# Performance work log

Hardware: AMD Instinct MI355X
Metric: run time of the kernel (lower is better)

## Reference

```python
import jax, jax.numpy as jnp
import numpy as np
from jax import lax

B, C, H, W = 4, 256, 64, 64
K = 9          # points
G = 32         # GroupNorm groups
EPS = 1e-5


def base_offset():
    # matches get_base_offset: y = 0, x in [-(K-1)//2 .. K//2], interleaved (y,x)
    bx = jnp.arange(-((K - 1) // 2), K // 2 + 1, dtype=jnp.float32)
    by = jnp.zeros_like(bx)
    return jnp.stack([by, bx], axis=1).reshape(1, 2 * K, 1, 1)


def conv3x3(x, w, b):
    y = lax.conv_general_dilated(x, w, (1, 1), ((1, 1), (1, 1)),
                                 dimension_numbers=('NCHW', 'OIHW', 'NCHW'))
    return y + b[None, :, None, None]


def group_norm(x, gamma, beta):
    b, c, h, w = x.shape
    xg = x.reshape(b, G, c // G, h, w)
    mu = xg.mean(axis=(2, 3, 4), keepdims=True)
    var = xg.var(axis=(2, 3, 4), keepdims=True)
    xn = ((xg - mu) * lax.rsqrt(var + EPS)).reshape(b, c, h, w)
    return xn * gamma[None, :, None, None] + beta[None, :, None, None]


def _deform_sample_one(img, off):
    # img: [C,H,W]; off: [K,2,H,W] (y,x). Kernel [1,K], stride 1, pad (0, K//2).
    c, h, w = img.shape
    base_x = (jnp.arange(K) - K // 2).astype(img.dtype)  # kernel grid x positions
    py = off[:, 0] + jnp.arange(h, dtype=img.dtype)[None, :, None]                 # [K,H,W]
    px = off[:, 1] + jnp.arange(w, dtype=img.dtype)[None, None, :] + base_x[:, None, None]
    y0 = jnp.floor(py)
    x0 = jnp.floor(px)
    wy = py - y0
    wx = px - x0
    flat = img.reshape(c, h * w)

    def corner(yi, xi):
        valid = (yi >= 0) & (yi <= h - 1) & (xi >= 0) & (xi <= w - 1)
        yc = jnp.clip(yi, 0, h - 1).astype(jnp.int32)
        xc = jnp.clip(xi, 0, w - 1).astype(jnp.int32)
        v = flat[:, (yc * w + xc).reshape(-1)].reshape(c, K, h, w)
        return v * valid[None].astype(img.dtype)

    return (corner(y0, x0) * ((1 - wy) * (1 - wx))[None]
            + corner(y0, x0 + 1) * ((1 - wy) * wx)[None]
            + corner(y0 + 1, x0) * (wy * (1 - wx))[None]
            + corner(y0 + 1, x0 + 1) * (wy * wx)[None])  # [C,K,H,W]


def deform_conv(x, offset, w):
    # x [B,C,H,W]; offset [B,2K,H,W]; w [O,C,1,K]; no bias (mmcv DeformConv2d)
    b, _, h, ww = x.shape
    off = offset.reshape(b, K, 2, h, ww)
    cols = jax.vmap(_deform_sample_one)(x, off)  # [B,C,K,H,W]
    return jnp.einsum('bckhw,ock->bohw', cols, w[:, :, 0, :])


def setup_inputs() -> dict:
    key = jax.random.key(0)
    ks = jax.random.split(key, 8)
    return {
        'cls_feat': jax.random.normal(ks[0], (B, C, H, W), jnp.float32),
        'reg_feat': jax.random.normal(ks[1], (B, C, H, W), jnp.float32),
        'offc_w': jax.random.normal(ks[2], (C, C, 3, 3), jnp.float32) * 0.01,
        'offc_b': jnp.zeros((C,), jnp.float32),
        'offc_g': jnp.ones((C,), jnp.float32),
        'offc_bt': jnp.zeros((C,), jnp.float32),
        'offo_w': jax.random.normal(ks[3], (2 * K, C, 3, 3), jnp.float32) * 0.01,
        'offo_b': jnp.zeros((2 * K,), jnp.float32),
        'clsdc_w': jax.random.normal(ks[4], (C, C, 1, K), jnp.float32) / np.sqrt(C * K),
        'cls_g': jnp.ones((C,), jnp.float32),
        'cls_bt': jnp.zeros((C,), jnp.float32),
        'regdc_w': jax.random.normal(ks[5], (C, C, 1, K), jnp.float32) / np.sqrt(C * K),
        'reg_g': jnp.ones((C,), jnp.float32),
        'reg_bt': jnp.zeros((C,), jnp.float32),
    }


def reference(cls_feat, reg_feat, offc_w, offc_b, offc_g, offc_bt,
              offo_w, offo_b, clsdc_w, cls_g, cls_bt, regdc_w, reg_g, reg_bt):
    # offset branch: ConvModule(3x3) -> GN -> ReLU, then 3x3 offset_out head
    t = jax.nn.relu(group_norm(conv3x3(reg_feat, offc_w, offc_b), offc_g, offc_bt))
    pts = conv3x3(t, offo_w, offo_b)          # [B, 2K, H, W]
    off = pts - base_offset()
    cls_out = jax.nn.relu(group_norm(deform_conv(cls_feat, off, clsdc_w), cls_g, cls_bt))
    reg_out = jax.nn.relu(group_norm(deform_conv(reg_feat, off, regdc_w), reg_g, reg_bt))
    return pts, cls_out, reg_out
```

## Files before the change

### kernel.cpp

```cpp
#include <hip/hip_runtime.h>
#include <math.h>

#define BB 4
#define CC 256
#define HH 64
#define WW 64
#define KP 9
#define GG 32
#define HWW (HH*WW)
#define FEL ((size_t)BB*CC*HH*WW)
#define GN_CNT 32768.0f

typedef __bf16 bf16x8 __attribute__((ext_vector_type(8)));
typedef float  f32x4  __attribute__((ext_vector_type(4)));
typedef float  f32x2  __attribute__((ext_vector_type(2)));

__device__ __forceinline__ float bflo(unsigned u) {
    union { unsigned u; float f; } x; x.u = u << 16; return x.f;
}
__device__ __forceinline__ float bfhi(unsigned u) {
    union { unsigned u; float f; } x; x.u = u & 0xffff0000u; return x.f;
}
__device__ __forceinline__ f32x2 up2(unsigned u) {
    return (f32x2){bflo(u), bfhi(u)};
}

#define VT256_RD(row, P)  (((row) << 8) + ((((P) ^ ((row) & 7))) << 3))
#define VT128_RD(row, P)  (((row) << 7) + ((((P) ^ ((row) & 7))) << 3))

__global__ void prep_and_transpose(
    const float* __restrict__ cls, const float* __restrict__ reg,
    __bf16* __restrict__ out_cls, __bf16* __restrict__ out_reg,
    const float* __restrict__ w1, const float* __restrict__ wc,
    const float* __restrict__ wr, const float* __restrict__ w18,
    __bf16* __restrict__ f1, __bf16* __restrict__ fc,
    __bf16* __restrict__ fr, __bf16* __restrict__ f18,
    float* __restrict__ stats)
{
    int blk = blockIdx.x;
    if (blk < 2048) {
        __shared__ float tile[64][65];
        int c0 = (blk & 3) * 64;
        int y  = (blk >> 2) & 63;
        int z  = blk >> 8;
        int b  = z & 3;
        const float* in = (z >> 2) ? reg : cls;
        __bf16* out     = (z >> 2) ? out_reg : out_cls;
        int lx = threadIdx.x & 63;
        int q  = threadIdx.x >> 6;
        for (int j = 0; j < 16; ++j) {
            int ci = q * 16 + j;
            tile[ci][lx] = in[(((size_t)b*CC + c0 + ci)*HH + y)*WW + lx];
        }
        __syncthreads();
        for (int j = 0; j < 16; ++j) {
            int xi = q * 16 + j;
            out[(((size_t)b*HH + y)*WW + xi)*CC + c0 + lx] = (__bf16)tile[lx][xi];
        }
        return;
    }
    int gid = (blk - 2048) * 256 + threadIdx.x;
    if (gid < 768) stats[gid] = 0.f;
    const int NW = 589824;
    if (gid < 3 * NW) {
        int which = gid / NW;
        int idx = gid - which * NW;
        int j   = idx & 7;
        int l   = (idx >> 3) & 63;
        int o16 = (idx >> 9) & 15;
        int c0  = (idx >> 13) & 7;
        int k   = idx >> 16;
        int o = o16 * 16 + (l & 15);
        int c = c0 * 32 + (l >> 4) * 8 + j;
        const float* src = (which == 0) ? w1 : ((which == 1) ? wc : wr);
        __bf16* dst = (which == 0) ? f1 : ((which == 1) ? fc : fr);
        dst[idx] = (__bf16)src[(size_t)(o * 256 + c) * 9 + k];
    } else {
        int idx = gid - 3 * NW;
        int j   = idx & 7;
        int l   = (idx >> 3) & 63;
        int o16 = (idx >> 9) & 1;
        int c0  = (idx >> 10) & 7;
        int k   = idx >> 13;
        int o = o16 * 16 + (l & 15);
        int c = c0 * 32 + (l >> 4) * 8 + j;
        float v = (o < 18) ? w18[(size_t)(o * 256 + c) * 9 + k] : 0.f;
        f18[idx] = (__bf16)v;
    }
}

__global__ __launch_bounds__(256, 4) void conv1_mfma(
    const __bf16* __restrict__ in_cl,
    const __bf16* __restrict__ wf,
    const float* __restrict__ bias,
    __bf16* __restrict__ t_out,
    float* __restrict__ stats)
{
    __shared__ __bf16 Vt[66 * 256];
    __shared__ float groupStats[64];
    int blk = blockIdx.x;
    int bb = blk & 3;
    int oq = (blk >> 2) & 3;
    int y  = blk >> 4;
    int t  = threadIdx.x;
    int w  = t >> 6;
    int l  = t & 63;
    int quad = l >> 4;
    int l15  = l & 15;
    if (t < 64) groupStats[t] = 0.f;

    const __bf16* inb = in_cl + (size_t)bb * HWW * CC;
    f32x4 acc[4];
    #pragma unroll
    for (int i = 0; i < 4; ++i) acc[i] = (f32x4){0.f, 0.f, 0.f, 0.f};

    for (int ky = 0; ky < 3; ++ky) {
        int yy = y + ky - 1;
        bool yok = (yy >= 0 && yy < HH);
        __syncthreads();
        for (int u = t; u < 66 * 32; u += 256) {
            int xl = u >> 5, cu = u & 31;
            int gx = xl - 1;
            uint4 val = make_uint4(0u, 0u, 0u, 0u);
            if (yok && gx >= 0 && gx < WW)
                val = *(const uint4*)(inb + ((size_t)(yy * WW + gx)) * CC + cu * 8);
            *(uint4*)&Vt[VT256_RD(xl, cu)] = val;
        }
        __syncthreads();
        #pragma unroll
        for (int kx = 0; kx < 3; ++kx) {
            int k = ky * 3 + kx;
            const bf16x8* wbase = (const bf16x8*)(wf + (size_t)k * 65536);
            for (int c0 = 0; c0 < 8; ++c0) {
                bf16x8 a[4];
                #pragma unroll
                for (int pt = 0; pt < 4; ++pt) {
                    int row = pt * 16 + l15 + kx;
                    a[pt] = *(const bf16x8*)&Vt[VT256_RD(row, c0 * 4 + quad)];
                }
                bf16x8 bfr = wbase[(c0 * 16 + (oq * 4 + w)) * 64 + l];
                #pragma unroll
                for (int pt = 0; pt < 4; ++pt)
                    acc[pt] = __builtin_amdgcn_mfma_f32_16x16x32_bf16(
                        a[pt], bfr, acc[pt], 0, 0, 0);
            }
        }
    }
    {
        int o = oq * 64 + w * 16 + l15;
        float bi = bias[o];
        float s1 = 0.f, s2 = 0.f;
        #pragma unroll
        for (int pt = 0; pt < 4; ++pt)
            #pragma unroll
            for (int r = 0; r < 4; ++r) {
                float v = acc[pt][r] + bi;
                int px = pt * 16 + quad * 4 + r;
                t_out[(((size_t)bb * HH + y) * WW + px) * CC + o] = (__bf16)v;
                s1 += v; s2 += v * v;
            }
        s1 += __shfl_xor(s1, 16, 64); s1 += __shfl_xor(s1, 32, 64);
        s2 += __shfl_xor(s2, 16, 64); s2 += __shfl_xor(s2, 32, 64);
        if (quad == 0) {
            atomicAdd(&groupStats[(o >> 3) * 2],     s1);
            atomicAdd(&groupStats[(o >> 3) * 2 + 1], s2);
        }
    }
    __syncthreads();
    if (t < 64) atomicAdd(&stats[bb * 64 + t], groupStats[t]);
}

__global__ __launch_bounds__(256, 4) void conv18_mfma(
    const __bf16* __restrict__ t_bf,
    const __bf16* __restrict__ wf18,
    const float* __restrict__ bias,
    const float* __restrict__ stats,
    const float* __restrict__ gamma, const float* __restrict__ beta,
    float* __restrict__ pts)
{
    __shared__ __bf16 Vt[34 * 256];
    int blk = blockIdx.x;
    int bb = blk & 3;
    int xh = (blk >> 2) & 1;
    int y  = blk >> 3;
    int t  = threadIdx.x;
    int w  = t >> 6;
    int l  = t & 63;
    int quad = l >> 4;
    int l15  = l & 15;
    int mt   = w & 1;
    int o16  = w >> 1;
    int x0   = xh * 32;
    const __bf16* inb = t_bf + (size_t)bb * HWW * CC;

    int cu = t & 31;
    int cbase = cu * 8;
    float mu = stats[bb * 64 + cu * 2]     * (1.f / GN_CNT);
    float ms = stats[bb * 64 + cu * 2 + 1] * (1.f / GN_CNT);
    float rs = rsqrtf(ms - mu * mu + 1e-5f);
    float sc[8], sh[8];
    #pragma unroll
    for (int j = 0; j < 8; ++j) {
        float ga = gamma[cbase + j];
        sc[j] = rs * ga;
        sh[j] = beta[cbase + j] - mu * rs * ga;
    }

    f32x4 acc = (f32x4){0.f, 0.f, 0.f, 0.f};

    for (int ky = 0; ky < 3; ++ky) {
        int yy = y + ky - 1;
        bool yok = (yy >= 0 && yy < HH);
        __syncthreads();
        for (int u = t; u < 34 * 32; u += 256) {
            int xl = u >> 5;
            int gx = x0 - 1 + xl;
            uint4 val = make_uint4(0u, 0u, 0u, 0u);
            if (yok && gx >= 0 && gx < WW) {
                uint4 q = *(const uint4*)(inb + ((size_t)(yy * WW + gx)) * CC + cu * 8);
                __bf16 o8[8];
                unsigned qq[4] = {q.x, q.y, q.z, q.w};
                #pragma unroll
                for (int h = 0; h < 4; ++h) {
                    float lo = fmaxf(bflo(qq[h]) * sc[h*2]   + sh[h*2],   0.f);
                    float hi = fmaxf(bfhi(qq[h]) * sc[h*2+1] + sh[h*2+1], 0.f);
                    o8[h*2]   = (__bf16)lo;
                    o8[h*2+1] = (__bf16)hi;
                }
                val = *(const uint4*)o8;
            }
            *(uint4*)&Vt[VT256_RD(xl, cu)] = val;
        }
        __syncthreads();
        #pragma unroll
        for (int kx = 0; kx < 3; ++kx) {
            int k = ky * 3 + kx;
            const bf16x8* wbase = (const bf16x8*)(wf18 + (size_t)k * 8192);
            for (int c0 = 0; c0 < 8; ++c0) {
                int row = mt * 16 + l15 + kx;
                bf16x8 a = *(const bf16x8*)&Vt[VT256_RD(row, c0 * 4 + quad)];
                bf16x8 bfr = wbase[(c0 * 2 + o16) * 64 + l];
                acc = __builtin_amdgcn_mfma_f32_16x16x32_bf16(a, bfr, acc, 0, 0, 0);
            }
        }
    }
    {
        int o = o16 * 16 + l15;
        if (o < 18) {
            float bi = bias[o];
            float4 st;
            st.x = acc[0] + bi;
            st.y = acc[1] + bi;
            st.z = acc[2] + bi;
            st.w = acc[3] + bi;
            *(float4*)(pts + (((size_t)bb*18 + o)*HH + y)*WW + x0 + mt*16 + quad*4) = st;
        }
    }
}

__global__ __launch_bounds__(512, 4) void deform_mfma(
    const __bf16* __restrict__ cls_cl, const __bf16* __restrict__ reg_cl,
    const __bf16* __restrict__ wfc, const __bf16* __restrict__ wfr,
    const float* __restrict__ pts,
    __bf16* __restrict__ out_cls, __bf16* __restrict__ out_reg,
    float* __restrict__ stats)
{
    __shared__ float pairW4[576 * 4];
    __shared__ int   pairO4[576 * 4];
    __shared__ __bf16 Vt[2][64 * 128];
    __shared__ float groupStats[64];

    int blk = blockIdx.x;
    int g8  = blk & 7;
    int which = g8 & 1;
    int bb  = g8 >> 1;
    int y   = blk >> 3;
    const __bf16* featb = (which ? reg_cl : cls_cl) + (size_t)bb * HWW * CC;
    const __bf16* wf    = which ? wfr : wfc;
    __bf16* outp  = which ? out_reg : out_cls;
    float* statsP = stats + 256 + which * 256 + bb * 64;

    int t = threadIdx.x;
    int w = t >> 6;
    int l = t & 63;
    int quad = l >> 4;
    int l15  = l & 15;
    int cq4  = t & 15;
    int pxg  = t >> 4;

    if (t < 64) groupStats[t] = 0.f;
    for (int j = t; j < 576; j += 512) {
        int k = j >> 6;
        int x = j & 63;
        float py  = pts[(((size_t)bb*18 + 2*k)*HH + y)*WW + x] + (float)y;
        float pxf = pts[(((size_t)bb*18 + 2*k + 1)*HH + y)*WW + x] + (float)x;
        float y0f = floorf(py), x0f = floorf(pxf);
        float wy = py - y0f, wx = pxf - x0f;
        int iy0 = (int)y0f, ix0 = (int)x0f;
        int iy1 = iy0 + 1,  ix1 = ix0 + 1;
        bool vy0 = (iy0 >= 0 && iy0 < HH), vy1 = (iy1 >= 0 && iy1 < HH);
        bool vx0 = (ix0 >= 0 && ix0 < WW), vx1 = (ix1 >= 0 && ix1 < WW);
        int cy0 = min(max(iy0, 0), HH-1), cy1 = min(max(iy1, 0), HH-1);
        int cx0 = min(max(ix0, 0), WW-1), cx1 = min(max(ix1, 0), WW-1);
        pairW4[j*4+0] = (1.f-wy)*(1.f-wx) * ((vy0 && vx0) ? 1.f : 0.f);
        pairW4[j*4+1] = (1.f-wy)*wx       * ((vy0 && vx1) ? 1.f : 0.f);
        pairW4[j*4+2] = wy*(1.f-wx)       * ((vy1 && vx0) ? 1.f : 0.f);
        pairW4[j*4+3] = wy*wx             * ((vy1 && vx1) ? 1.f : 0.f);
        pairO4[j*4+0] = (cy0*WW + cx0)*CC;
        pairO4[j*4+1] = (cy0*WW + cx1)*CC;
        pairO4[j*4+2] = (cy1*WW + cx0)*CC;
        pairO4[j*4+3] = (cy1*WW + cx1)*CC;
    }

    f32x4 acc[2][4];
    #pragma unroll
    for (int i = 0; i < 2; ++i)
        #pragma unroll
        for (int j = 0; j < 4; ++j)
            acc[i][j] = (f32x4){0.f, 0.f, 0.f, 0.f};

    uint4 L[2][4];

    auto gathers = [&](int s) {
        int k = s >> 1, ch = s & 1;
        const __bf16* fb = featb + ch * 128 + cq4 * 8;
        #pragma unroll
        for (int it = 0; it < 2; ++it) {
            int j = k * 64 + it * 32 + pxg;
            int4 ov = *(const int4*)&pairO4[j * 4];
            L[it][0] = *(const uint4*)(fb + ov.x);
            L[it][1] = *(const uint4*)(fb + ov.y);
            L[it][2] = *(const uint4*)(fb + ov.z);
            L[it][3] = *(const uint4*)(fb + ov.w);
        }
    };
    auto combine = [&](int s) {
        __bf16* buf = &Vt[s & 1][0];
        int k = s >> 1;
        #pragma unroll
        for (int it = 0; it < 2; ++it) {
            int pxi = it * 32 + pxg;
            float4 wv = *(const float4*)&pairW4[(k * 64 + pxi) * 4];
            __bf16 o8[8];
            unsigned q0[4] = {L[it][0].x, L[it][0].y, L[it][0].z, L[it][0].w};
            unsigned q1[4] = {L[it][1].x, L[it][1].y, L[it][1].z, L[it][1].w};
            unsigned q2[4] = {L[it][2].x, L[it][2].y, L[it][2].z, L[it][2].w};
            unsigned q3[4] = {L[it][3].x, L[it][3].y, L[it][3].z, L[it][3].w};
            #pragma unroll
            for (int h = 0; h < 4; ++h) {
                f32x2 r = wv.x * up2(q0[h]);
                r += wv.y * up2(q1[h]);
                r += wv.z * up2(q2[h]);
                r += wv.w * up2(q3[h]);
                o8[h*2]   = (__bf16)r.x;
                o8[h*2+1] = (__bf16)r.y;
            }
            *(uint4*)&buf[VT128_RD(pxi, cq4)] = *(const uint4*)o8;
        }
    };
    auto stage_mfma = [&](int s) {
        int ch = s & 1;
        const __bf16* buf = &Vt[s & 1][0];
        const bf16x8* wbase = (const bf16x8*)(wf + (size_t)(s >> 1) * 65536);
        #pragma unroll
        for (int u = 0; u < 4; ++u) {
            bf16x8 a[4], bfr[2];
            #pragma unroll
            for (int pt = 0; pt < 4; ++pt)
                a[pt] = *(const bf16x8*)&buf[VT128_RD(pt * 16 + l15, u * 4 + quad)];
            #pragma unroll
            for (int ot = 0; ot < 2; ++ot)
                bfr[ot] = wbase[(((ch * 4 + u) * 16) + (w * 2 + ot)) * 64 + l];
            #pragma unroll
            for (int ot = 0; ot < 2; ++ot)
                #pragma unroll
                for (int pt = 0; pt < 4; ++pt)
                    acc[ot][pt] = __builtin_amdgcn_mfma_f32_16x16x32_bf16(
                        bfr[ot], a[pt], acc[ot][pt], 0, 0, 0);
        }
    };

    __syncthreads();
    gathers(0);
    combine(0);
    #pragma unroll 1
    for (int s = 1; s < 18; ++s) {
        __syncthreads();
        gathers(s);
        stage_mfma(s - 1);
        combine(s);
    }
    __syncthreads();
    stage_mfma(17);

    #pragma unroll
    for (int ot = 0; ot < 2; ++ot) {
        float s1 = 0.f, s2 = 0.f;
        #pragma unroll
        for (int r = 0; r < 4; ++r) {
            int o = w * 32 + ot * 16 + quad * 4 + r;
            __bf16* orow = outp + ((size_t)(bb*CC + o))*HWW + y*WW + l15;
            #pragma unroll
            for (int pt = 0; pt < 4; ++pt) {
                float v = acc[ot][pt][r];
                orow[pt * 16] = (__bf16)v;
                s1 += v; s2 += v * v;
            }
        }
        s1 += __shfl_xor(s1, 1, 64); s1 += __shfl_xor(s1, 2, 64);
        s1 += __shfl_xor(s1, 4, 64); s1 += __shfl_xor(s1, 8, 64);
        s1 += __shfl_xor(s1, 16, 64);
        s2 += __shfl_xor(s2, 1, 64); s2 += __shfl_xor(s2, 2, 64);
        s2 += __shfl_xor(s2, 4, 64); s2 += __shfl_xor(s2, 8, 64);
        s2 += __shfl_xor(s2, 16, 64);
        if ((l & 31) == 0) {
            int g = w * 4 + ot * 2 + (l >> 5);
            atomicAdd(&groupStats[g * 2],     s1);
            atomicAdd(&groupStats[g * 2 + 1], s2);
        }
    }
    __syncthreads();
    if (t < 64) atomicAdd(&statsP[t], groupStats[t]);
}

__global__ void gn_relu_nchw(const __bf16* __restrict__ in_cls, const __bf16* __restrict__ in_reg,
                             float* __restrict__ out_cls, float* __restrict__ out_reg,
                             const float* __restrict__ stats_base,
                             const float* __restrict__ gcls, const float* __restrict__ bcls,
                             const float* __restrict__ greg, const float* __restrict__ breg) {
    int which = blockIdx.y;
    const __bf16* in = which ? in_reg  : in_cls;
    float* out       = which ? out_reg : out_cls;
    const float* st  = stats_base + (which ? 512 : 256);
    const float* gg  = which ? greg : gcls;
    const float* be  = which ? breg : bcls;
    size_t e = ((size_t)blockIdx.x * 256 + threadIdx.x) * 8;
    int c = (int)((e >> 12) & 255);
    int b = (int)(e >> 20);
    int g = c >> 3;
    float mu = st[(b*32 + g)*2] * (1.f / GN_CNT);
    float ms = st[(b*32 + g)*2 + 1] * (1.f / GN_CNT);
    float rs = rsqrtf(ms - mu*mu + 1e-5f);
    float ga = gg[c], bb = be[c];
    uint4 q = *(const uint4*)(in + e);
    float v[8] = {bflo(q.x), bfhi(q.x), bflo(q.y), bfhi(q.y),
                  bflo(q.z), bfhi(q.z), bflo(q.w), bfhi(q.w)};
    float4 r0, r1;
    r0.x = fmaxf((v[0] - mu)*rs*ga + bb, 0.f);
    r0.y = fmaxf((v[1] - mu)*rs*ga + bb, 0.f);
    r0.z = fmaxf((v[2] - mu)*rs*ga + bb, 0.f);
    r0.w = fmaxf((v[3] - mu)*rs*ga + bb, 0.f);
    r1.x = fmaxf((v[4] - mu)*rs*ga + bb, 0.f);
    r1.y = fmaxf((v[5] - mu)*rs*ga + bb, 0.f);
    r1.z = fmaxf((v[6] - mu)*rs*ga + bb, 0.f);
    r1.w = fmaxf((v[7] - mu)*rs*ga + bb, 0.f);
    *(float4*)(out + e)     = r0;
    *(float4*)(out + e + 4) = r1;
}

extern "C" void kernel_launch(void* const* d_in, const int* in_sizes, int n_in,
                              void* d_out, int out_size, void* d_ws, size_t ws_size,
                              hipStream_t stream) {
    (void)in_sizes; (void)n_in; (void)out_size; (void)ws_size;
    const float* cls_feat = (const float*)d_in[0];
    const float* reg_feat = (const float*)d_in[1];
    const float* offc_w   = (const float*)d_in[2];
    const float* offc_b   = (const float*)d_in[3];
    const float* offc_g   = (const float*)d_in[4];
    const float* offc_bt  = (const float*)d_in[5];
    const float* offo_w   = (const float*)d_in[6];
    const float* offo_b   = (const float*)d_in[7];
    const float* clsdc_w  = (const float*)d_in[8];
    const float* cls_g    = (const float*)d_in[9];
    const float* cls_bt   = (const float*)d_in[10];
    const float* regdc_w  = (const float*)d_in[11];
    const float* reg_g    = (const float*)d_in[12];
    const float* reg_bt   = (const float*)d_in[13];
    float* out = (float*)d_out;

    char* ws = (char*)d_ws;
    __bf16* reg_cl = (__bf16*)ws;
    __bf16* cls_cl = (__bf16*)(ws + 8388608);
    __bf16* t_bf   = (__bf16*)(ws + 16777216);
    __bf16* dc_cls = (__bf16*)(ws + 25165824);
    __bf16* dc_reg = (__bf16*)(ws + 33554432);
    __bf16* wt1f   = (__bf16*)(ws + 41943040);
    __bf16* wtcf   = (__bf16*)(ws + 41943040 + 1179648);
    __bf16* wtrf   = (__bf16*)(ws + 41943040 + 2359296);
    __bf16* wf18   = (__bf16*)(ws + 41943040 + 3538944);
    float*  stats  = (float*)(ws + 41943040 + 3686400);

    float* pts     = out;
    float* out_cls = out + 294912;
    float* out_reg = out + 294912 + FEL;

    hipLaunchKernelGGL(prep_and_transpose, dim3(9248), dim3(256), 0, stream,
                       cls_feat, reg_feat, cls_cl, reg_cl,
                       offc_w, clsdc_w, regdc_w, offo_w,
                       wt1f, wtcf, wtrf, wf18, stats);
    hipLaunchKernelGGL(conv1_mfma, dim3(1024), dim3(256), 0, stream,
                       reg_cl, wt1f, offc_b, t_bf, stats);
    hipLaunchKernelGGL(conv18_mfma, dim3(512), dim3(256), 0, stream,
                       t_bf, wf18, offo_b, stats, offc_g, offc_bt, pts);
    hipLaunchKernelGGL(deform_mfma, dim3(512), dim3(512), 0, stream,
                       cls_cl, reg_cl, wtcf, wtrf, pts, dc_cls, dc_reg, stats);
    hipLaunchKernelGGL(gn_relu_nchw, dim3(2048, 2), dim3(256), 0, stream,
                       dc_cls, dc_reg, out_cls, out_reg,
                       stats, cls_g, cls_bt, reg_g, reg_bt);
}
```

Before: 230.4 us.

## Widen conv1 and deform blocks to cover all channels and two rows

Measured after the change: 239.8 us. 4.1% more time.

```diff
diff --git a/kernel.cpp b/kernel.cpp
--- a/kernel.cpp
+++ b/kernel.cpp
@@ -89,7 +89,7 @@
     }
 }
 
-__global__ __launch_bounds__(256, 4) void conv1_mfma(
+__global__ __launch_bounds__(512, 2) void conv1_mfma(
     const __bf16* __restrict__ in_cl,
     const __bf16* __restrict__ wf,
     const float* __restrict__ bias,
@@ -100,8 +100,7 @@
     __shared__ float groupStats[64];
     int blk = blockIdx.x;
     int bb = blk & 3;
-    int oq = (blk >> 2) & 3;
-    int y  = blk >> 4;
+    int y  = blk >> 2;
     int t  = threadIdx.x;
     int w  = t >> 6;
     int l  = t & 63;
@@ -110,15 +109,18 @@
     if (t < 64) groupStats[t] = 0.f;
 
     const __bf16* inb = in_cl + (size_t)bb * HWW * CC;
-    f32x4 acc[4];
+    f32x4 acc[4][2];
     #pragma unroll
-    for (int i = 0; i < 4; ++i) acc[i] = (f32x4){0.f, 0.f, 0.f, 0.f};
+    for (int i = 0; i < 4; ++i)
+        #pragma unroll
+        for (int j = 0; j < 2; ++j)
+            acc[i][j] = (f32x4){0.f, 0.f, 0.f, 0.f};
 
     for (int ky = 0; ky < 3; ++ky) {
         int yy = y + ky - 1;
         bool yok = (yy >= 0 && yy < HH);
         __syncthreads();
-        for (int u = t; u < 66 * 32; u += 256) {
+        for (int u = t; u < 66 * 32; u += 512) {
             int xl = u >> 5, cu = u & 31;
             int gx = xl - 1;
             uint4 val = make_uint4(0u, 0u, 0u, 0u);
@@ -132,29 +134,34 @@
             int k = ky * 3 + kx;
             const bf16x8* wbase = (const bf16x8*)(wf + (size_t)k * 65536);
             for (int c0 = 0; c0 < 8; ++c0) {
-                bf16x8 a[4];
+                bf16x8 a[4], bfr[2];
                 #pragma unroll
                 for (int pt = 0; pt < 4; ++pt) {
                     int row = pt * 16 + l15 + kx;
                     a[pt] = *(const bf16x8*)&Vt[VT256_RD(row, c0 * 4 + quad)];
                 }
-                bf16x8 bfr = wbase[(c0 * 16 + (oq * 4 + w)) * 64 + l];
+                #pragma unroll
+                for (int ot = 0; ot < 2; ++ot)
+                    bfr[ot] = wbase[(c0 * 16 + (w * 2 + ot)) * 64 + l];
                 #pragma unroll
                 for (int pt = 0; pt < 4; ++pt)
-                    acc[pt] = __builtin_amdgcn_mfma_f32_16x16x32_bf16(
-                        a[pt], bfr, acc[pt], 0, 0, 0);
-            }
-        }
-    }
-    {
-        int o = oq * 64 + w * 16 + l15;
+                    #pragma unroll
+                    for (int ot = 0; ot < 2; ++ot)
+                        acc[pt][ot] = __builtin_amdgcn_mfma_f32_16x16x32_bf16(
+                            a[pt], bfr[ot], acc[pt][ot], 0, 0, 0);
+            }
+        }
+    }
+    #pragma unroll
+    for (int ot = 0; ot < 2; ++ot) {
+        int o = w * 32 + ot * 16 + l15;
         float bi = bias[o];
         float s1 = 0.f, s2 = 0.f;
         #pragma unroll
         for (int pt = 0; pt < 4; ++pt)
             #pragma unroll
             for (int r = 0; r < 4; ++r) {
-                float v = acc[pt][r] + bi;
+                float v = acc[pt][ot][r] + bi;
                 int px = pt * 16 + quad * 4 + r;
                 t_out[(((size_t)bb * HH + y) * WW + px) * CC + o] = (__bf16)v;
                 s1 += v; s2 += v * v;
@@ -258,23 +265,23 @@
     }
 }
 
-__global__ __launch_bounds__(512, 4) void deform_mfma(
+__global__ __launch_bounds__(1024, 1) void deform_mfma(
     const __bf16* __restrict__ cls_cl, const __bf16* __restrict__ reg_cl,
     const __bf16* __restrict__ wfc, const __bf16* __restrict__ wfr,
     const float* __restrict__ pts,
     __bf16* __restrict__ out_cls, __bf16* __restrict__ out_reg,
     float* __restrict__ stats)
 {
-    __shared__ float pairW4[576 * 4];
-    __shared__ int   pairO4[576 * 4];
-    __shared__ __bf16 Vt[2][64 * 128];
+    __shared__ float pairW4[1152 * 4];
+    __shared__ int   pairO4[1152 * 4];
+    __shared__ __bf16 Vt[2][128 * 128];
     __shared__ float groupStats[64];
 
     int blk = blockIdx.x;
     int g8  = blk & 7;
     int which = g8 & 1;
     int bb  = g8 >> 1;
-    int y   = blk >> 3;
+    int y0  = (blk >> 3) * 2;
     const __bf16* featb = (which ? reg_cl : cls_cl) + (size_t)bb * HWW * CC;
     const __bf16* wf    = which ? wfr : wfc;
     __bf16* outp  = which ? out_reg : out_cls;
@@ -286,12 +293,17 @@
     int quad = l >> 4;
     int l15  = l & 15;
     int cq4  = t & 15;
-    int pxg  = t >> 4;
+    int sg   = t >> 4;
+    int ow   = w & 7;
+    int rh   = w >> 3;
 
     if (t < 64) groupStats[t] = 0.f;
-    for (int j = t; j < 576; j += 512) {
-        int k = j >> 6;
-        int x = j & 63;
+    for (int j = t; j < 1152; j += 1024) {
+        int k = j >> 7;
+        int site = j & 127;
+        int r = site >> 6;
+        int x = site & 63;
+        int y = y0 + r;
         float py  = pts[(((size_t)bb*18 + 2*k)*HH + y)*WW + x] + (float)y;
         float pxf = pts[(((size_t)bb*18 + 2*k + 1)*HH + y)*WW + x] + (float)x;
         float y0f = floorf(py), x0f = floorf(pxf);
@@ -326,7 +338,7 @@
         const __bf16* fb = featb + ch * 128 + cq4 * 8;
         #pragma unroll
         for (int it = 0; it < 2; ++it) {
-            int j = k * 64 + it * 32 + pxg;
+            int j = k * 128 + it * 64 + sg;
             int4 ov = *(const int4*)&pairO4[j * 4];
             L[it][0] = *(const uint4*)(fb + ov.x);
             L[it][1] = *(const uint4*)(fb + ov.y);
@@ -339,8 +351,8 @@
         int k = s >> 1;
         #pragma unroll
         for (int it = 0; it < 2; ++it) {
-            int pxi = it * 32 + pxg;
-            float4 wv = *(const float4*)&pairW4[(k * 64 + pxi) * 4];
+            int site = it * 64 + sg;
+            float4 wv = *(const float4*)&pairW4[(k * 128 + site) * 4];
             __bf16 o8[8];
             unsigned q0[4] = {L[it][0].x, L[it][0].y, L[it][0].z, L[it][0].w};
             unsigned q1[4] = {L[it][1].x, L[it][1].y, L[it][1].z, L[it][1].w};
@@ -355,7 +367,7 @@
                 o8[h*2]   = (__bf16)r.x;
                 o8[h*2+1] = (__bf16)r.y;
             }
-            *(uint4*)&buf[VT128_RD(pxi, cq4)] = *(const uint4*)o8;
+            *(uint4*)&buf[VT128_RD(site, cq4)] = *(const uint4*)o8;
         }
     };
     auto stage_mfma = [&](int s) {
@@ -366,11 +378,13 @@
         for (int u = 0; u < 4; ++u) {
             bf16x8 a[4], bfr[2];
             #pragma unroll
-            for (int pt = 0; pt < 4; ++pt)
-                a[pt] = *(const bf16x8*)&buf[VT128_RD(pt * 16 + l15, u * 4 + quad)];
+            for (int pt = 0; pt < 4; ++pt) {
+                int row = rh * 64 + pt * 16 + l15;
+                a[pt] = *(const bf16x8*)&buf[VT128_RD(row, u * 4 + quad)];
+            }
             #pragma unroll
             for (int ot = 0; ot < 2; ++ot)
-                bfr[ot] = wbase[(((ch * 4 + u) * 16) + (w * 2 + ot)) * 64 + l];
+                bfr[ot] = wbase[(((ch * 4 + u) * 16) + (ow * 2 + ot)) * 64 + l];
             #pragma unroll
             for (int ot = 0; ot < 2; ++ot)
                 #pragma unroll
@@ -398,8 +412,8 @@
         float s1 = 0.f, s2 = 0.f;
         #pragma unroll
         for (int r = 0; r < 4; ++r) {
-            int o = w * 32 + ot * 16 + quad * 4 + r;
-            __bf16* orow = outp + ((size_t)(bb*CC + o))*HWW + y*WW + l15;
+            int o = ow * 32 + ot * 16 + quad * 4 + r;
+            __bf16* orow = outp + ((size_t)(bb*CC + o))*HWW + (y0 + rh)*WW + l15;
             #pragma unroll
             for (int pt = 0; pt < 4; ++pt) {
                 float v = acc[ot][pt][r];
@@ -414,7 +428,7 @@
         s2 += __shfl_xor(s2, 4, 64); s2 += __shfl_xor(s2, 8, 64);
         s2 += __shfl_xor(s2, 16, 64);
         if ((l & 31) == 0) {
-            int g = w * 4 + ot * 2 + (l >> 5);
+            int g = ow * 4 + ot * 2 + (l >> 5);
             atomicAdd(&groupStats[g * 2],     s1);
             atomicAdd(&groupStats[g * 2 + 1], s2);
         }
@@ -498,11 +512,11 @@
                        cls_feat, reg_feat, cls_cl, reg_cl,
                        offc_w, clsdc_w, regdc_w, offo_w,
                        wt1f, wtcf, wtrf, wf18, stats);
-    hipLaunchKernelGGL(conv1_mfma, dim3(1024), dim3(256), 0, stream,
+    hipLaunchKernelGGL(conv1_mfma, dim3(256), dim3(512), 0, stream,
                        reg_cl, wt1f, offc_b, t_bf, stats);
     hipLaunchKernelGGL(conv18_mfma, dim3(512), dim3(256), 0, stream,
                        t_bf, wf18, offo_b, stats, offc_g, offc_bt, pts);
-    hipLaunchKernelGGL(deform_mfma, dim3(512), dim3(512), 0, stream,
+    hipLaunchKernelGGL(deform_mfma, dim3(256), dim3(1024), 0, stream,
                        cls_cl, reg_cl, wtcf, wtrf, pts, dc_cls, dc_reg, stats);
     hipLaunchKernelGGL(gn_relu_nchw, dim3(2048, 2), dim3(256), 0, stream,
                        dc_cls, dc_reg, out_cls, out_reg,
```

## Retile conv1 MFMA warps to 2x2 pixel/output tiles and widen LDS swizzle

Applied to the files above, without the earlier changes.

New measurement: 233.3 us. Within noise of the previous version (+1.2%).

```diff
diff --git a/kernel.cpp b/kernel.cpp
--- a/kernel.cpp
+++ b/kernel.cpp
@@ -25,8 +25,8 @@
     return (f32x2){bflo(u), bfhi(u)};
 }
 
-#define VT256_RD(row, P)  (((row) << 8) + ((((P) ^ ((row) & 7))) << 3))
-#define VT128_RD(row, P)  (((row) << 7) + ((((P) ^ ((row) & 7))) << 3))
+#define VT256_RD(row, P)  (((row) << 8) + ((((P) ^ ((row) & 15))) << 3))
+#define VT128_RD(row, P)  (((row) << 7) + ((((P) ^ ((row) & 15))) << 3))
 
 __global__ void prep_and_transpose(
     const float* __restrict__ cls, const float* __restrict__ reg,
@@ -107,12 +107,17 @@
     int l  = t & 63;
     int quad = l >> 4;
     int l15  = l & 15;
+    int ph  = w & 1;
+    int oh2 = w >> 1;
     if (t < 64) groupStats[t] = 0.f;
 
     const __bf16* inb = in_cl + (size_t)bb * HWW * CC;
-    f32x4 acc[4];
+    f32x4 acc[2][2];
     #pragma unroll
-    for (int i = 0; i < 4; ++i) acc[i] = (f32x4){0.f, 0.f, 0.f, 0.f};
+    for (int i = 0; i < 2; ++i)
+        #pragma unroll
+        for (int j = 0; j < 2; ++j)
+            acc[i][j] = (f32x4){0.f, 0.f, 0.f, 0.f};
 
     for (int ky = 0; ky < 3; ++ky) {
         int yy = y + ky - 1;
@@ -132,30 +137,35 @@
             int k = ky * 3 + kx;
             const bf16x8* wbase = (const bf16x8*)(wf + (size_t)k * 65536);
             for (int c0 = 0; c0 < 8; ++c0) {
-                bf16x8 a[4];
+                bf16x8 a[2], bfr[2];
                 #pragma unroll
-                for (int pt = 0; pt < 4; ++pt) {
-                    int row = pt * 16 + l15 + kx;
+                for (int pt = 0; pt < 2; ++pt) {
+                    int row = ph * 32 + pt * 16 + l15 + kx;
                     a[pt] = *(const bf16x8*)&Vt[VT256_RD(row, c0 * 4 + quad)];
                 }
-                bf16x8 bfr = wbase[(c0 * 16 + (oq * 4 + w)) * 64 + l];
                 #pragma unroll
-                for (int pt = 0; pt < 4; ++pt)
-                    acc[pt] = __builtin_amdgcn_mfma_f32_16x16x32_bf16(
-                        a[pt], bfr, acc[pt], 0, 0, 0);
+                for (int ot = 0; ot < 2; ++ot)
+                    bfr[ot] = wbase[(c0 * 16 + (oq * 4 + oh2 * 2 + ot)) * 64 + l];
+                #pragma unroll
+                for (int pt = 0; pt < 2; ++pt)
+                    #pragma unroll
+                    for (int ot = 0; ot < 2; ++ot)
+                        acc[pt][ot] = __builtin_amdgcn_mfma_f32_16x16x32_bf16(
+                            a[pt], bfr[ot], acc[pt][ot], 0, 0, 0);
             }
         }
     }
-    {
-        int o = oq * 64 + w * 16 + l15;
+    #pragma unroll
+    for (int ot = 0; ot < 2; ++ot) {
+        int o = oq * 64 + oh2 * 32 + ot * 16 + l15;
         float bi = bias[o];
         float s1 = 0.f, s2 = 0.f;
         #pragma unroll
-        for (int pt = 0; pt < 4; ++pt)
+        for (int pt = 0; pt < 2; ++pt)
             #pragma unroll
             for (int r = 0; r < 4; ++r) {
-                float v = acc[pt][r] + bi;
-                int px = pt * 16 + quad * 4 + r;
+                float v = acc[pt][ot][r] + bi;
+                int px = ph * 32 + pt * 16 + quad * 4 + r;
                 t_out[(((size_t)bb * HH + y) * WW + px) * CC + o] = (__bf16)v;
                 s1 += v; s2 += v * v;
             }
```
